# Performance work log

Measured on AMD Instinct MI355X. Metric: run time of the kernel, lower is better.

## Reference

```python
import jax, jax.numpy as jnp
import numpy as np

B, C, D_EMB = 512, 100000, 128
SCALE = 3.0
EPS = 1e-5


def _l2norm(x, eps=1e-12):
    # matches torch F.normalize(p=2, dim=-1)
    n = jnp.sqrt(jnp.sum(x * x, axis=-1, keepdims=True))
    return x / jnp.maximum(n, eps)


def setup_inputs() -> dict:
    key = jax.random.key(0)
    k1, k2, k3 = jax.random.split(key, 3)
    X = jax.random.normal(k1, (B, D_EMB), dtype=jnp.float32)
    indices = jnp.arange(B, dtype=jnp.int64)
    T = jax.random.randint(k2, (B,), 0, C).astype(jnp.int64)
    proxies = jax.random.normal(k3, (C, D_EMB), dtype=jnp.float32) / 8.0
    return {"X": X, "indices": indices, "T": T, "proxies": proxies}


def reference(X, indices, T, proxies):
    P = _l2norm(proxies)            # (C, D)
    Xn = _l2norm(X)                 # (B, D)

    # cross_attention -----------------------------------------------------
    Pb = P[T]                       # (B, D) gather of class proxies
    # affinity2boundary[b,k] = relu(<(Pb[b]+Pb[k])/2, Xn[k]>)
    #   = relu(0.5 * ((Pb @ Xn.T)[b,k] + diag[k]))  -- avoids (B,B,D) intermediate
    diag = jnp.sum(Pb * Xn, axis=-1)                       # (B,)
    aff2b = jax.nn.relu(0.5 * (Pb @ Xn.T + diag[None, :]))  # (B, B)
    aff2x = jax.nn.relu(Xn @ Xn.T)                          # (B, B)
    attention = aff2b + aff2x

    # NOTE: faithful to torch broadcasting: (B,B) / (B,) divides by COLUMN sums
    attention = attention / (attention.sum(-1) + EPS)       # (B, B)
    attention_weights = attention @ Xn                      # (B, D)
    X2 = Xn + attention_weights

    Ps = SCALE * _l2norm(P)         # (C, D), rows have norm SCALE
    Xs = SCALE * _l2norm(X2)        # (B, D)

    # squared pairwise distance block between X rows and proxy rows
    sx = jnp.sum(Xs * Xs, axis=-1)  # (B,)
    sp = jnp.sum(Ps * Ps, axis=-1)  # (C,)
    Dm = jnp.maximum(sx[:, None] + sp[None, :] - 2.0 * (Xs @ Ps.T), 0.0)  # (B, C)

    # one-hot targets (smoothing_const = 0) with masked log-softmax
    lsm = jax.nn.log_softmax(-Dm, axis=-1)                  # (B, C)
    loss = -lsm[jnp.arange(B), T]                           # (B,)
    return loss.mean()
```

## Files before the change

### kernel.cpp

```cpp
#include <hip/hip_runtime.h>
#include <hip/hip_bf16.h>
#include <math.h>

#define B_N 512
#define C_N 100000
#define CPAD 100032
#define D_N 128
#define NCHUNK (CPAD / 64)
#define K5_BLOCKS (CPAD / 4)
#define K6_GX 256
#define K6_GY 2
#define K6_BLOCKS (K6_GX * K6_GY)
#define PAD_CORR (32.0f * 1.522998e-8f)

typedef short short8 __attribute__((ext_vector_type(8)));
typedef float f32x4 __attribute__((ext_vector_type(4)));

__device__ __forceinline__ unsigned short f2bf(float f) {
  unsigned int u = __float_as_uint(f);
  u += 0x7fffu + ((u >> 16) & 1u);
  return (unsigned short)(u >> 16);
}

__device__ __forceinline__ void gl_lds16(const void* g, void* l) {
  __builtin_amdgcn_global_load_lds(
      (const __attribute__((address_space(1))) void*)g,
      (__attribute__((address_space(3))) void*)l, 16, 0, 0);
}

template <int NT>
__device__ __forceinline__ float block_reduce_sum(float v, float* red) {
  int t = threadIdx.x;
  __syncthreads();
  red[t] = v;
  __syncthreads();
#pragma unroll
  for (int s = NT / 2; s > 0; s >>= 1) {
    if (t < s) red[t] += red[t + s];
    __syncthreads();
  }
  return red[0];
}

__global__ __launch_bounds__(256) void kA(const float* __restrict__ X,
                                          const float* __restrict__ proxies,
                                          const int* __restrict__ T,
                                          float* __restrict__ Xn, float* __restrict__ Pb,
                                          float* __restrict__ diagv, float* __restrict__ X2,
                                          unsigned short* __restrict__ Pnb) {
  int bid = blockIdx.x;
  int t = threadIdx.x;
  if (bid < K5_BLOCKS) {
    int lane = t & 63;
    int row = bid * 4 + (t >> 6);
    float2 v = make_float2(0.f, 0.f);
    if (row < C_N) v = *(const float2*)(proxies + (size_t)row * D_N + 2 * lane);
    float ss = v.x * v.x + v.y * v.y;
#pragma unroll
    for (int off = 1; off < 64; off <<= 1) ss += __shfl_xor(ss, off);
    float inv = 1.f / fmaxf(sqrtf(ss), 1e-12f);
    unsigned short a = f2bf(v.x * inv), b = f2bf(v.y * inv);
    unsigned int pk = (unsigned int)a | ((unsigned int)b << 16);
    *(unsigned int*)(Pnb + (size_t)row * D_N + 2 * lane) = pk;
  } else {
    __shared__ float red[256];
    int b = bid - K5_BLOCKS;
    bool act = t < D_N;
    float v = act ? X[b * D_N + t] : 0.f;
    float ss = block_reduce_sum<256>(v * v, red);
    float xn = v / fmaxf(sqrtf(ss), 1e-12f);
    if (act) {
      Xn[b * D_N + t] = xn;
      X2[b * D_N + t] = 0.f;
    }
    int row = T[b];
    float p = act ? proxies[(size_t)row * D_N + t] : 0.f;
    float ss2 = block_reduce_sum<256>(p * p, red);
    float pn = p / fmaxf(sqrtf(ss2), 1e-12f);
    if (act) Pb[b * D_N + t] = pn;
    float d = block_reduce_sum<256>(pn * xn, red);
    if (t == 0) diagv[b] = d;
  }
}

__global__ __launch_bounds__(256) void k3_att(const float* __restrict__ Xn,
                                              const float* __restrict__ Pb,
                                              const float* __restrict__ diagv,
                                              float* __restrict__ A, float* __restrict__ S) {
  __shared__ float xb[128], pbv[128];
  __shared__ float red[256];
  int b = blockIdx.x, t = threadIdx.x;
  if (t < 128) {
    xb[t] = Xn[b * D_N + t];
    pbv[t] = Pb[b * D_N + t];
  }
  __syncthreads();
  float rs = 0.f;
  for (int k = t; k < B_N; k += 256) {
    const float4* xr = (const float4*)(Xn + (size_t)k * D_N);
    float d1 = 0.f, d2 = 0.f;
#pragma unroll
    for (int i = 0; i < 32; i++) {
      float4 v = xr[i];
      d1 += pbv[4 * i] * v.x + pbv[4 * i + 1] * v.y + pbv[4 * i + 2] * v.z + pbv[4 * i + 3] * v.w;
      d2 += xb[4 * i] * v.x + xb[4 * i + 1] * v.y + xb[4 * i + 2] * v.z + xb[4 * i + 3] * v.w;
    }
    float a = fmaxf(0.5f * (d1 + diagv[k]), 0.f) + fmaxf(d2, 0.f);
    A[(size_t)b * B_N + k] = a;
    rs += a;
  }
  rs = block_reduce_sum<256>(rs, red);
  if (t == 0) S[b] = rs;
}

__global__ void k4a_aw(const float* __restrict__ Xn, const float* __restrict__ A,
                       const float* __restrict__ S, float* __restrict__ X2) {
  __shared__ float aw[128];
  int b = blockIdx.x, t = threadIdx.x;
  int k0 = blockIdx.y * 128;
  aw[t] = A[(size_t)b * B_N + k0 + t] / (S[k0 + t] + 1e-5f);
  __syncthreads();
  float acc = 0.f;
#pragma unroll 16
  for (int kk = 0; kk < 128; kk++) acc += aw[kk] * Xn[(size_t)(k0 + kk) * D_N + t];
  atomicAdd(&X2[b * D_N + t], acc);
}

__global__ void k4b_xs(const float* __restrict__ Xn, const float* __restrict__ X2,
                       const float* __restrict__ Pb, unsigned short* __restrict__ Xsb,
                       float* __restrict__ lossT, float* __restrict__ sumexpP,
                       int* __restrict__ ctrs) {
  __shared__ float red[128];
  int b = blockIdx.x, t = threadIdx.x;
  float x2 = Xn[b * D_N + t] + X2[b * D_N + t];
  float ss = block_reduce_sum<128>(x2 * x2, red);
  float xs = 3.f * x2 / fmaxf(sqrtf(ss), 1e-12f);
  Xsb[b * D_N + t] = f2bf(xs);
  float dt = block_reduce_sum<128>(xs * Pb[b * D_N + t], red);
  if (t == 0) {
    lossT[b] = fmaxf(18.f - 6.f * dt, 0.f);
    sumexpP[b * 16] = 0.f;
    if (b == 0) ctrs[32] = 0;
  }
}

__global__ __launch_bounds__(256, 2) void k6_big(const unsigned short* __restrict__ Pnb,
                                                 const unsigned short* __restrict__ Xsb,
                                                 float* __restrict__ sumexpP,
                                                 const float* __restrict__ lossT,
                                                 int* __restrict__ ctrs,
                                                 float* __restrict__ out) {
  __shared__ __align__(16) unsigned short sP[2][64 * 128];
  __shared__ float redf[256];
  __shared__ int sLast;
  const int t = threadIdx.x;
  const int w = t >> 6;
  const int lane = t & 63;
  const int lc = lane & 15;
  const int q = lane >> 4;
  const int b0 = blockIdx.y * 256;

  short8 afr[4][4];
#pragma unroll
  for (int mt = 0; mt < 4; mt++)
#pragma unroll
    for (int ks = 0; ks < 4; ks++)
      afr[mt][ks] = *(const short8*)(Xsb + (size_t)(b0 + 64 * w + 16 * mt + lc) * D_N +
                                     ks * 32 + q * 8);

  float pe[4][4];
#pragma unroll
  for (int mt = 0; mt < 4; mt++)
#pragma unroll
    for (int r = 0; r < 4; r++) pe[mt][r] = 0.f;

  const int rR = 16 * w + (lane >> 4);
  const int gsrc0 = (lane & 15);
#define STAGE(c0_, buf_)                                                              \
  {                                                                                   \
    _Pragma("unroll") for (int j = 0; j < 4; j++) {                                   \
      int R = rR + 4 * j;                                                             \
      int g = gsrc0 ^ ((R)&15);                                                       \
      gl_lds16(Pnb + (((size_t)(c0_) + R) << 7) + (g << 3),                           \
               &sP[buf_][w * 2048 + j * 512]);                                        \
    }                                                                                 \
  }

  int cc = blockIdx.x;
  STAGE(cc * 64, 0);
  int buf = 0;
  while (true) {
    int nc = cc + gridDim.x;
    if (nc < NCHUNK) STAGE(nc * 64, buf ^ 1);
    __builtin_amdgcn_sched_barrier(0);
    __builtin_amdgcn_s_waitcnt(0x0F74);
    __builtin_amdgcn_s_barrier();
    __builtin_amdgcn_sched_barrier(0);

    f32x4 acc[4][4];
#pragma unroll
    for (int mt = 0; mt < 4; mt++)
#pragma unroll
      for (int nt = 0; nt < 4; nt++) acc[mt][nt] = (f32x4){0.f, 0.f, 0.f, 0.f};

#pragma unroll
    for (int ks = 0; ks < 4; ks++) {
      short8 bfr[4];
#pragma unroll
      for (int nt = 0; nt < 4; nt++) {
        int R = 16 * nt + lc;
        int g = (ks * 4 + q) ^ lc;
        bfr[nt] = *(const short8*)(&sP[buf][R * 128 + (g << 3)]);
      }
#pragma unroll
      for (int nt = 0; nt < 4; nt++)
#pragma unroll
        for (int mt = 0; mt < 4; mt++)
          acc[mt][nt] = __builtin_amdgcn_mfma_f32_16x16x32_bf16(afr[mt][ks], bfr[nt],
                                                                acc[mt][nt], 0, 0, 0);
    }

#pragma unroll
    for (int mt = 0; mt < 4; mt++)
#pragma unroll
      for (int nt = 0; nt < 4; nt++) {
        f32x4 a = acc[mt][nt];
#pragma unroll
        for (int r = 0; r < 4; r++)
          pe[mt][r] += __expf(fminf(__fmaf_rn(6.f, a[r], -18.f), 0.f));
      }

    if (nc >= NCHUNK) break;
    __builtin_amdgcn_sched_barrier(0);
    __builtin_amdgcn_s_barrier();
    cc = nc;
    buf ^= 1;
  }

#pragma unroll
  for (int mt = 0; mt < 4; mt++) {
#pragma unroll
    for (int r = 0; r < 4; r++) {
      float p = pe[mt][r];
      p += __shfl_xor(p, 1);
      p += __shfl_xor(p, 2);
      p += __shfl_xor(p, 4);
      p += __shfl_xor(p, 8);
      if (lc == 0) {
        int rb = b0 + 64 * w + 16 * mt + 4 * q + r;
        atomicAdd(&sumexpP[rb * 16], p);
      }
    }
  }

  __builtin_amdgcn_s_waitcnt(0);
  if (t == 0) sLast = atomicAdd(&ctrs[32], 1);
  __syncthreads();
  if (sLast == K6_BLOCKS - 1) {
    float v = 0.f;
#pragma unroll
    for (int i = 0; i < 2; i++) {
      int b = t + 256 * i;
      float se = __hip_atomic_load(&sumexpP[b * 16], __ATOMIC_RELAXED,
                                   __HIP_MEMORY_SCOPE_AGENT);
      v += lossT[b] + logf(se - PAD_CORR);
    }
    float s = block_reduce_sum<256>(v, redf);
    if (t == 0) out[0] = s * (1.0f / 512.0f);
  }
}

extern "C" void kernel_launch(void* const* d_in, const int* in_sizes, int n_in,
                              void* d_out, int out_size, void* d_ws, size_t ws_size,
                              hipStream_t stream) {
  const float* X = (const float*)d_in[0];
  const int* T = (const int*)d_in[2];
  const float* proxies = (const float*)d_in[3];
  float* out = (float*)d_out;

  char* ws = (char*)d_ws;
  unsigned short* Pnb = (unsigned short*)ws;
  float* Xn = (float*)(ws + (size_t)CPAD * D_N * 2);
  float* Pb = Xn + B_N * D_N;
  float* X2 = Pb + B_N * D_N;
  float* dg = X2 + B_N * D_N;
  float* S = dg + B_N;
  float* lossT = S + B_N;
  float* sumexpP = lossT + B_N;
  unsigned short* Xsb = (unsigned short*)(sumexpP + B_N * 16);
  float* A = (float*)(Xsb + B_N * D_N);
  int* ctrs = (int*)(A + B_N * B_N);

  kA<<<K5_BLOCKS + B_N, 256, 0, stream>>>(X, proxies, T, Xn, Pb, dg, X2, Pnb);
  k3_att<<<B_N, 256, 0, stream>>>(Xn, Pb, dg, A, S);
  k4a_aw<<<dim3(B_N, 4), 128, 0, stream>>>(Xn, A, S, X2);
  k4b_xs<<<B_N, 128, 0, stream>>>(Xn, X2, Pb, Xsb, lossT, sumexpP, ctrs);
  k6_big<<<dim3(K6_GX, K6_GY), 256, 0, stream>>>(Pnb, Xsb, sumexpP, lossT, ctrs, out);
}
```

Measured before the change: 160.5 us.

## Fuse attention kernels with an in-kernel grid barrier and use exp2

Merges the attention score, column-normalised weighted sum and Xs normalisation kernels into one kernel. The row scores stay in shared memory, and the column sums are exchanged through a global atomic-counter grid barrier. This removes two kernel launches, the global A matrix round trip and the X2 atomics. It relies on all 512 blocks being co-resident, which risks deadlock if they are not. Separately, the k6 exponent is rewritten as exp2 with prescaled constants to save a multiply per element.

```diff
diff --git a/kernel.cpp b/kernel.cpp
--- a/kernel.cpp
+++ b/kernel.cpp
@@ -46,8 +46,9 @@
                                           const float* __restrict__ proxies,
                                           const int* __restrict__ T,
                                           float* __restrict__ Xn, float* __restrict__ Pb,
-                                          float* __restrict__ diagv, float* __restrict__ X2,
-                                          unsigned short* __restrict__ Pnb) {
+                                          float* __restrict__ diagv,
+                                          unsigned short* __restrict__ Pnb,
+                                          int* __restrict__ ctrs) {
   int bid = blockIdx.x;
   int t = threadIdx.x;
   if (bid < K5_BLOCKS) {
@@ -69,25 +70,30 @@
     float v = act ? X[b * D_N + t] : 0.f;
     float ss = block_reduce_sum<256>(v * v, red);
     float xn = v / fmaxf(sqrtf(ss), 1e-12f);
-    if (act) {
-      Xn[b * D_N + t] = xn;
-      X2[b * D_N + t] = 0.f;
-    }
+    if (act) Xn[b * D_N + t] = xn;
     int row = T[b];
     float p = act ? proxies[(size_t)row * D_N + t] : 0.f;
     float ss2 = block_reduce_sum<256>(p * p, red);
     float pn = p / fmaxf(sqrtf(ss2), 1e-12f);
     if (act) Pb[b * D_N + t] = pn;
     float d = block_reduce_sum<256>(pn * xn, red);
-    if (t == 0) diagv[b] = d;
-  }
-}
-
-__global__ __launch_bounds__(256) void k3_att(const float* __restrict__ Xn,
-                                              const float* __restrict__ Pb,
-                                              const float* __restrict__ diagv,
-                                              float* __restrict__ A, float* __restrict__ S) {
+    if (t == 0) {
+      diagv[b] = d;
+      if (b == 0) ctrs[64] = 0;
+    }
+  }
+}
+
+__global__ __launch_bounds__(256, 2) void kB_att(const float* __restrict__ Xn,
+                                                 const float* __restrict__ Pb,
+                                                 const float* __restrict__ diagv,
+                                                 float* __restrict__ Sg,
+                                                 unsigned short* __restrict__ Xsb,
+                                                 float* __restrict__ lossT,
+                                                 float* __restrict__ sumexpP,
+                                                 int* __restrict__ ctrs) {
   __shared__ float xb[128], pbv[128];
+  __shared__ float aL[512];
   __shared__ float red[256];
   int b = blockIdx.x, t = threadIdx.x;
   if (t < 128) {
@@ -95,6 +101,7 @@
     pbv[t] = Pb[b * D_N + t];
   }
   __syncthreads();
+
   float rs = 0.f;
   for (int k = t; k < B_N; k += 256) {
     const float4* xr = (const float4*)(Xn + (size_t)k * D_N);
@@ -106,37 +113,42 @@
       d2 += xb[4 * i] * v.x + xb[4 * i + 1] * v.y + xb[4 * i + 2] * v.z + xb[4 * i + 3] * v.w;
     }
     float a = fmaxf(0.5f * (d1 + diagv[k]), 0.f) + fmaxf(d2, 0.f);
-    A[(size_t)b * B_N + k] = a;
+    aL[k] = a;
     rs += a;
   }
   rs = block_reduce_sum<256>(rs, red);
-  if (t == 0) S[b] = rs;
-}
-
-__global__ void k4a_aw(const float* __restrict__ Xn, const float* __restrict__ A,
-                       const float* __restrict__ S, float* __restrict__ X2) {
-  __shared__ float aw[128];
-  int b = blockIdx.x, t = threadIdx.x;
-  int k0 = blockIdx.y * 128;
-  aw[t] = A[(size_t)b * B_N + k0 + t] / (S[k0 + t] + 1e-5f);
-  __syncthreads();
-  float acc = 0.f;
-#pragma unroll 16
-  for (int kk = 0; kk < 128; kk++) acc += aw[kk] * Xn[(size_t)(k0 + kk) * D_N + t];
-  atomicAdd(&X2[b * D_N + t], acc);
-}
-
-__global__ void k4b_xs(const float* __restrict__ Xn, const float* __restrict__ X2,
-                       const float* __restrict__ Pb, unsigned short* __restrict__ Xsb,
-                       float* __restrict__ lossT, float* __restrict__ sumexpP,
-                       int* __restrict__ ctrs) {
-  __shared__ float red[128];
-  int b = blockIdx.x, t = threadIdx.x;
-  float x2 = Xn[b * D_N + t] + X2[b * D_N + t];
-  float ss = block_reduce_sum<128>(x2 * x2, red);
+
+  if (t == 0) {
+    __hip_atomic_store(&Sg[b], rs, __ATOMIC_RELAXED, __HIP_MEMORY_SCOPE_AGENT);
+    __builtin_amdgcn_s_waitcnt(0);
+    atomicAdd(&ctrs[64], 1);
+    while (__hip_atomic_load(&ctrs[64], __ATOMIC_RELAXED, __HIP_MEMORY_SCOPE_AGENT) < B_N)
+      __builtin_amdgcn_s_sleep(2);
+  }
+  __syncthreads();
+  __builtin_amdgcn_sched_barrier(0);
+
+  for (int k = t; k < B_N; k += 256) {
+    float sv = __hip_atomic_load(&Sg[k], __ATOMIC_RELAXED, __HIP_MEMORY_SCOPE_AGENT);
+    aL[k] = aL[k] / (sv + 1e-5f);
+  }
+  __syncthreads();
+  int d = t & 127, h = t >> 7;
+  const float* xp = Xn + (size_t)(256 * h) * D_N + d;
+  float acc0 = 0.f, acc1 = 0.f;
+#pragma unroll 4
+  for (int kk = 0; kk < 256; kk += 2) {
+    acc0 = fmaf(aL[256 * h + kk], xp[(size_t)kk * D_N], acc0);
+    acc1 = fmaf(aL[256 * h + kk + 1], xp[(size_t)(kk + 1) * D_N], acc1);
+  }
+  red[t] = acc0 + acc1;
+  __syncthreads();
+  float x2 = (t < 128) ? (xb[t] + red[t] + red[t + 128]) : 0.f;
+
+  float ss = block_reduce_sum<256>(x2 * x2, red);
   float xs = 3.f * x2 / fmaxf(sqrtf(ss), 1e-12f);
-  Xsb[b * D_N + t] = f2bf(xs);
-  float dt = block_reduce_sum<128>(xs * Pb[b * D_N + t], red);
+  if (t < 128) Xsb[b * D_N + t] = f2bf(xs);
+  float dt = block_reduce_sum<256>((t < 128) ? xs * pbv[t] : 0.f, red);
   if (t == 0) {
     lossT[b] = fmaxf(18.f - 6.f * dt, 0.f);
     sumexpP[b * 16] = 0.f;
@@ -227,7 +239,8 @@
         f32x4 a = acc[mt][nt];
 #pragma unroll
         for (int r = 0; r < 4; r++)
-          pe[mt][r] += __expf(fminf(__fmaf_rn(6.f, a[r], -18.f), 0.f));
+          pe[mt][r] += __builtin_amdgcn_exp2f(
+              fminf(__fmaf_rn(8.65617024533378f, a[r], -25.9685107360013f), 0.f));
       }
 
     if (nc >= NCHUNK) break;
@@ -291,9 +304,7 @@
   float* A = (float*)(Xsb + B_N * D_N);
   int* ctrs = (int*)(A + B_N * B_N);
 
-  kA<<<K5_BLOCKS + B_N, 256, 0, stream>>>(X, proxies, T, Xn, Pb, dg, X2, Pnb);
-  k3_att<<<B_N, 256, 0, stream>>>(Xn, Pb, dg, A, S);
-  k4a_aw<<<dim3(B_N, 4), 128, 0, stream>>>(Xn, A, S, X2);
-  k4b_xs<<<B_N, 128, 0, stream>>>(Xn, X2, Pb, Xsb, lossT, sumexpP, ctrs);
+  kA<<<K5_BLOCKS + B_N, 256, 0, stream>>>(X, proxies, T, Xn, Pb, dg, Pnb, ctrs);
+  kB_att<<<B_N, 256, 0, stream>>>(Xn, Pb, dg, S, Xsb, lossT, sumexpP, ctrs);
   k6_big<<<dim3(K6_GX, K6_GY), 256, 0, stream>>>(Pnb, Xsb, sumexpP, lossT, ctrs, out);
 }
```

Measured after the change: 186.5 us. 16.2% more time.
